# Optimization experiments

Measured on AMD Instinct MI355X. Metric: run time of the kernel, lower is better.

Reference implementation:

```python
import jax, jax.numpy as jnp
import numpy as np

N = 50000
E = 800000
NFEAT = 128
NHID = 64
NCLASS = 40


def setup_inputs() -> dict:
    key = jax.random.key(0)
    ks = jax.random.split(key, 12)
    return {
        "x": jax.random.normal(ks[0], (N, NFEAT), dtype=jnp.float32),
        "M": jax.random.uniform(ks[1], (N, 1), dtype=jnp.float32),
        "AM": jax.random.uniform(ks[2], (N, 1), dtype=jnp.float32),
        "adj_vals": jax.random.uniform(ks[3], (E,), dtype=jnp.float32),
        "adjZ_vals": jax.random.uniform(ks[4], (E,), dtype=jnp.float32),
        "W0": jax.random.normal(ks[5], (NFEAT, NFEAT), dtype=jnp.float32) * (1.414 / np.sqrt(NFEAT)),
        "b0": jnp.zeros((NFEAT,), dtype=jnp.float32),
        "W1": jax.random.normal(ks[6], (NFEAT, NHID), dtype=jnp.float32) * (1.414 / np.sqrt(NFEAT)),
        "b1": jnp.zeros((NHID,), dtype=jnp.float32),
        "W2": jax.random.normal(ks[7], (NHID, NCLASS), dtype=jnp.float32) * (1.0 / np.sqrt(NHID)),
        "b2": jnp.zeros((NCLASS,), dtype=jnp.float32),
        "row": jax.random.randint(ks[8], (E,), 0, N, dtype=jnp.int32),
        "col": jax.random.randint(ks[9], (E,), 0, N, dtype=jnp.int32),
    }


def _spmm(vals, row, col, X, n):
    # sparse (COO) @ dense: out[r] = sum_e vals[e] * X[col[e]] for row[e]==r
    return jax.ops.segment_sum(vals[:, None] * X[col], row, num_segments=n)


def reference(x, M, AM, adj_vals, adjZ_vals, W0, b0, W1, b1, W2, b2, row, col):
    n = x.shape[0]
    # gc0: PaGConv(nfeat->nfeat) on adjZ, then ReLU (dropout is identity in eval)
    h = _spmm(adjZ_vals, row, col, M * x, n) * AM
    h = jax.nn.relu(h @ W0 + b0)
    # gc1: PaGConv(nfeat->nhid) on adjZ, then ReLU
    h = _spmm(adjZ_vals, row, col, M * h, n) * AM
    h = jax.nn.relu(h @ W1 + b1)
    # gc2: plain GConv(nhid->nclass) on adj
    h = _spmm(adj_vals, row, col, h, n)
    h = h @ W2 + b2
    return jax.nn.log_softmax(h, axis=1)
```

## Files before the change

### kernel.cpp

```cpp
#include <hip/hip_runtime.h>
#include <hip/hip_bf16.h>
#include <math.h>


typedef __attribute__((ext_vector_type(8))) short bf16x8;
typedef __attribute__((ext_vector_type(4))) float f32x4;

#define HIST_EPB_LOG 14
#define HIST_EPB 16384
#define NBINS 50176

__device__ __forceinline__ float rl_f(float v, int j) {
    return __builtin_bit_cast(float,
        __builtin_amdgcn_readlane(__builtin_bit_cast(int, v), j));
}
__device__ __forceinline__ int rl_i(int v, int j) {
    return __builtin_amdgcn_readlane(v, j);
}
__device__ __forceinline__ unsigned short f2bf(float f) {
    unsigned u = __builtin_bit_cast(unsigned, f);
    u += 0x7fffu + ((u >> 16) & 1u);
    return (unsigned short)(u >> 16);
}
__device__ __forceinline__ unsigned pack2bf(float lo, float hi) {
    return (unsigned)f2bf(lo) | ((unsigned)f2bf(hi) << 16);
}
__device__ __forceinline__ float bf_lo(unsigned u) {
    return __builtin_bit_cast(float, u << 16);
}
__device__ __forceinline__ float bf_hi(unsigned u) {
    return __builtin_bit_cast(float, u & 0xffff0000u);
}
__device__ __forceinline__ float clampf(float v) {
    return fminf(fmaxf(v, -1e30f), 1e30f);
}


__global__ void prep_wt(const float* __restrict__ W0, const float* __restrict__ W1,
                        const float* __restrict__ W2,
                        unsigned short* __restrict__ wt0, unsigned short* __restrict__ wt1,
                        unsigned short* __restrict__ wt2) {
    int idx = blockIdx.x * 256 + threadIdx.x;
    if (idx < 128 * 128) {
        int nn = idx >> 7, k = idx & 127;
        wt0[idx] = f2bf(W0[k * 128 + nn]);
    }
    idx -= 128 * 128;
    if (idx >= 0 && idx < 64 * 128) {
        int nn = idx >> 7, k = idx & 127;
        wt1[idx] = f2bf(W1[k * 64 + nn]);
    }
    idx -= 64 * 128;
    if (idx >= 0 && idx < 48 * 64) {
        int nn = idx >> 6, k = idx & 63;
        wt2[idx] = (nn < 40) ? f2bf(W2[k * 40 + nn]) : (unsigned short)0;
    }
}


template <int K, int COLS, int NTPAD, bool ABF16, bool MSCALE>
__device__ __forceinline__ void gemm_mfma_body(const void* __restrict__ Asrc,
                                               const float* __restrict__ Mv,
                                               const unsigned short* __restrict__ Wt,
                                               unsigned short* __restrict__ outp,
                                               int n, int bid, int tid) {
    constexpr int KS = K / 32;
    const int lane = tid & 63;
    const int wid = tid >> 6;
    const int m15 = lane & 15;
    const int q = lane >> 4;
    const int rA = bid * 64 + wid * 16 + m15;

    bf16x8 a[KS];
    if constexpr (ABF16) {
        const unsigned short* A = (const unsigned short*)Asrc;
#pragma unroll
        for (int ks = 0; ks < KS; ++ks) {
            uint4 z = make_uint4(0u, 0u, 0u, 0u);
            if (rA < n) z = *(const uint4*)(A + (size_t)rA * K + ks * 32 + q * 8);
            a[ks] = __builtin_bit_cast(bf16x8, z);
        }
    } else {
        const float* A = (const float*)Asrc;
        float m = 1.0f;
        if constexpr (MSCALE) { if (rA < n) m = Mv[rA]; }
#pragma unroll
        for (int ks = 0; ks < KS; ++ks) {
            float4 lo = make_float4(0.f, 0.f, 0.f, 0.f);
            float4 hi = make_float4(0.f, 0.f, 0.f, 0.f);
            if (rA < n) {
                lo = *(const float4*)(A + (size_t)rA * K + ks * 32 + q * 8);
                hi = *(const float4*)(A + (size_t)rA * K + ks * 32 + q * 8 + 4);
            }
            union { bf16x8 v; unsigned short u[8]; } pk;
            pk.u[0] = f2bf(lo.x * m); pk.u[1] = f2bf(lo.y * m);
            pk.u[2] = f2bf(lo.z * m); pk.u[3] = f2bf(lo.w * m);
            pk.u[4] = f2bf(hi.x * m); pk.u[5] = f2bf(hi.y * m);
            pk.u[6] = f2bf(hi.z * m); pk.u[7] = f2bf(hi.w * m);
            a[ks] = pk.v;
        }
    }

#pragma unroll
    for (int nt = 0; nt < NTPAD / 16; ++nt) {
        f32x4 acc = {0.f, 0.f, 0.f, 0.f};
        const int bn = nt * 16 + m15;
#pragma unroll
        for (int ks = 0; ks < KS; ++ks) {
            const uint4 z = *(const uint4*)(Wt + (size_t)bn * K + ks * 32 + q * 8);
            const bf16x8 b = __builtin_bit_cast(bf16x8, z);
            acc = __builtin_amdgcn_mfma_f32_16x16x32_bf16(a[ks], b, acc, 0, 0, 0);
        }
        const int gc = nt * 16 + m15;
#pragma unroll
        for (int rr = 0; rr < 4; ++rr) {
            const int gr = bid * 64 + wid * 16 + q * 4 + rr;
            bool ok = gr < n;
            if constexpr (NTPAD != COLS) ok = ok && (gc < COLS);
            if (ok) outp[(size_t)gr * COLS + gc] = f2bf(clampf(acc[rr]));
        }
    }
}

template <int K, int COLS, int NTPAD, bool ABF16, bool MSCALE>
__launch_bounds__(256)
__global__ void gemm_mfma(const void* __restrict__ A, const float* __restrict__ Mv,
                          const unsigned short* __restrict__ Wt,
                          unsigned short* __restrict__ out, int n) {
    gemm_mfma_body<K, COLS, NTPAD, ABF16, MSCALE>(A, Mv, Wt, out, n, blockIdx.x,
                                                  threadIdx.x);
}


__launch_bounds__(1024)
__global__ void hist_gemm0(const int* __restrict__ row,
                           unsigned short* __restrict__ cntmat,
                           unsigned short* __restrict__ lrank, int E, int NB,
                           const float* __restrict__ x, const float* __restrict__ Mv,
                           const unsigned short* __restrict__ Wt0,
                           unsigned short* __restrict__ t_buf, int n) {
    __shared__ unsigned hcnt[NBINS / 2];
    const int blk = blockIdx.x;
    const int t = threadIdx.x;
    if (blk < NB) {
        for (int i = t; i < NBINS / 2; i += 1024) hcnt[i] = 0u;
        __syncthreads();
        const int s = blk << HIST_EPB_LOG;
        const int e = min(E, s + HIST_EPB);
        for (int i = s + t; i < e; i += 1024) {
            const int r = row[i];
            const unsigned sh = (unsigned)(r & 1) << 4;
            const unsigned old = atomicAdd(&hcnt[r >> 1], 1u << sh);
            lrank[i] = (unsigned short)((old >> sh) & 0xffffu);
        }
        __syncthreads();
        unsigned* dst = (unsigned*)(cntmat + (size_t)blk * NBINS);
        for (int i = t; i < NBINS / 2; i += 1024) dst[i] = hcnt[i];
    } else {
        const int sub = t >> 8;
        gemm_mfma_body<128, 128, 128, false, true>(x, Mv, Wt0, t_buf, n,
                                                   (blk - NB) * 4 + sub, t & 255);
    }
}


__global__ void scan_part2(unsigned short* __restrict__ cm, int* __restrict__ rp,
                           int* __restrict__ bsums, int n, int NB) {
    __shared__ int sdata[256];
    const int t = threadIdx.x;
    const int base = blockIdx.x * 1024 + t * 4;
    unsigned r0 = 0, r1 = 0, r2 = 0, r3 = 0;
    for (int b = 0; b < NB; ++b) {
        uint2* p = (uint2*)&cm[(size_t)b * NBINS + base];
        const uint2 c = *p;
        uint2 o;
        o.x = r0 | (r1 << 16);
        o.y = r2 | (r3 << 16);
        *p = o;
        r0 += c.x & 0xffffu; r1 += c.x >> 16;
        r2 += c.y & 0xffffu; r3 += c.y >> 16;
    }
    int v[4] = {(int)r0, (int)r1, (int)r2, (int)r3};
    const int tsum = v[0] + v[1] + v[2] + v[3];
    sdata[t] = tsum;
    __syncthreads();
    for (int off = 1; off < 256; off <<= 1) {
        int xv = (t >= off) ? sdata[t - off] : 0;
        __syncthreads();
        sdata[t] += xv;
        __syncthreads();
    }
    int run = sdata[t] - tsum;
    if (t == 255) bsums[blockIdx.x] = sdata[t];
#pragma unroll
    for (int i = 0; i < 4; ++i) {
        if (base + i < n) rp[base + i] = run;
        run += v[i];
    }
}

__global__ void scan_top(int* __restrict__ bs, int nb) {
    int t = threadIdx.x;
    int orig = (t < nb) ? bs[t] : 0;
    int v = orig;
#pragma unroll
    for (int off = 1; off < 64; off <<= 1) {
        int x = __shfl_up(v, off);
        if (t >= off) v += x;
    }
    if (t < nb) bs[t] = v - orig;
}

__global__ void scan_add(int* __restrict__ rp, const int* __restrict__ bs,
                         int n, int total) {
    int i = blockIdx.x * blockDim.x + threadIdx.x;
    if (i < n) rp[i] += bs[i >> 10];
    if (i == 0) rp[n] = total;
}


__global__ void scatter_kernel(const int* __restrict__ row, const int* __restrict__ col,
                               const float* __restrict__ vA, const float* __restrict__ vZ,
                               const int* __restrict__ rp,
                               const unsigned short* __restrict__ cm,
                               const unsigned short* __restrict__ lrank,
                               float* __restrict__ packed, int E) {
    int e = blockIdx.x * blockDim.x + threadIdx.x;
    if (e >= E) return;
    const int r = row[e];
    const int pos = rp[r] + (int)cm[(size_t)(e >> HIST_EPB_LOG) * NBINS + r]
                          + (int)lrank[e];
    float3 pk;
    pk.x = __int_as_float(col[e]);
    pk.y = vZ[e];
    pk.z = vA[e];
    *(float3*)&packed[(size_t)3 * pos] = pk;
}


__launch_bounds__(256)
__global__ void spmm128_kernel(const float* __restrict__ packed,
                               const int* __restrict__ rp, const unsigned short* __restrict__ X,
                               const float* __restrict__ AM, const float* __restrict__ Mv,
                               const float* __restrict__ bias,
                               unsigned short* __restrict__ out, int n) {
    const int lane = threadIdx.x & 63;
    const int r = (int)((blockIdx.x * (unsigned)blockDim.x + threadIdx.x) >> 6);
    if (r >= n) return;
    const int s = __builtin_amdgcn_readfirstlane(rp[r]);
    const int e = __builtin_amdgcn_readfirstlane(rp[r + 1]);

    float acc0 = 0.0f, acc1 = 0.0f;
    for (int base = s; base < e; base += 64) {
        const int nn = min(64, e - base);
        int ci = 0; float vf = 0.0f;
        if (lane < nn) {
            const float3 pk = *(const float3*)&packed[(size_t)3 * (base + lane)];
            ci = __builtin_bit_cast(int, pk.x);
            vf = pk.y;
        }
        int j = 0;
        for (; j + 8 <= nn; j += 8) {
            unsigned u[8];
#pragma unroll
            for (int q = 0; q < 8; ++q) {
                const int cq = rl_i(ci, j + q);
                u[q] = *(const unsigned*)(X + (size_t)cq * 128 + lane * 2);
            }
#pragma unroll
            for (int q = 0; q < 8; ++q) {
                const float vq = rl_f(vf, j + q);
                acc0 += vq * bf_lo(u[q]);
                acc1 += vq * bf_hi(u[q]);
            }
        }
        for (; j < nn; ++j) {
            const int cq = rl_i(ci, j);
            const float vq = rl_f(vf, j);
            const unsigned u = *(const unsigned*)(X + (size_t)cq * 128 + lane * 2);
            acc0 += vq * bf_lo(u);
            acc1 += vq * bf_hi(u);
        }
    }

    const float am = AM[r];
    const float mr = Mv[r];
    const float o0 = fminf(fmaxf((acc0 * am + bias[2 * lane]) * mr, 0.0f), 1e30f);
    const float o1 = fminf(fmaxf((acc1 * am + bias[2 * lane + 1]) * mr, 0.0f), 1e30f);
    ((unsigned*)out)[(size_t)r * 64 + lane] = pack2bf(o0, o1);
}


__launch_bounds__(256)
__global__ void spmm64_kernel(const float* __restrict__ packed,
                              const int* __restrict__ rp, const unsigned short* __restrict__ X,
                              const float* __restrict__ AM, const float* __restrict__ bias,
                              unsigned short* __restrict__ out, int n) {
    const int lane = threadIdx.x & 63;
    const int g = lane >> 5;
    const int ls = lane & 31;
    const int r = (int)((blockIdx.x * (unsigned)blockDim.x + threadIdx.x) >> 6);
    if (r >= n) return;
    const int s = __builtin_amdgcn_readfirstlane(rp[r]);
    const int e = __builtin_amdgcn_readfirstlane(rp[r + 1]);

    float acc0 = 0.0f, acc1 = 0.0f;
    for (int base = s; base < e; base += 64) {
        const int nn = min(64, e - base);
        int ci = 0; float vf = 0.0f;
        if (lane < nn) {
            const float3 pk = *(const float3*)&packed[(size_t)3 * (base + lane)];
            ci = __builtin_bit_cast(int, pk.x);
            vf = pk.y;
        }
        for (int j = 0; j < nn; j += 8) {
#pragma unroll
            for (int q = 0; q < 4; ++q) {
                const int jj = j + 2 * q + g;
                const bool ok = jj < nn;
                const int idx = jj & 63;
                const int c = __shfl(ci, idx);
                const float v = __shfl(vf, idx);
                if (ok) {
                    const unsigned u = *(const unsigned*)(X + (size_t)c * 64 + ls * 2);
                    acc0 += v * bf_lo(u);
                    acc1 += v * bf_hi(u);
                }
            }
        }
    }
    acc0 += __shfl_xor(acc0, 32);
    acc1 += __shfl_xor(acc1, 32);

    if (lane < 32) {
        const float am = AM[r];
        const float o0 = fminf(fmaxf(acc0 * am + bias[2 * ls], 0.0f), 1e30f);
        const float o1 = fminf(fmaxf(acc1 * am + bias[2 * ls + 1], 0.0f), 1e30f);
        ((unsigned*)out)[(size_t)r * 32 + ls] = pack2bf(o0, o1);
    }
}


__launch_bounds__(256)
__global__ void spmm40_kernel(const float* __restrict__ packed,
                              const int* __restrict__ rp, const unsigned short* __restrict__ X,
                              const float* __restrict__ bias,
                              float* __restrict__ out, int n) {
    const int lane = threadIdx.x & 63;
    const int g = lane / 20;
    const int ls = lane - 20 * g;
    const bool active = g < 3;
    const int r = (int)((blockIdx.x * (unsigned)blockDim.x + threadIdx.x) >> 6);
    if (r >= n) return;
    const int s = __builtin_amdgcn_readfirstlane(rp[r]);
    const int e = __builtin_amdgcn_readfirstlane(rp[r + 1]);

    float acc0 = 0.0f, acc1 = 0.0f;
    for (int base = s; base < e; base += 64) {
        const int nn = min(64, e - base);
        int ci = 0; float vf = 0.0f;
        if (lane < nn) {
            const float3 pk = *(const float3*)&packed[(size_t)3 * (base + lane)];
            ci = __builtin_bit_cast(int, pk.x);
            vf = pk.z;
        }
        for (int j = 0; j < nn; j += 12) {
#pragma unroll
            for (int q = 0; q < 4; ++q) {
                const int jj = j + 3 * q + g;
                const bool ok = active && jj < nn;
                const int idx = jj & 63;
                const int c = __shfl(ci, idx);
                const float v = __shfl(vf, idx);
                if (ok) {
                    const unsigned u = *(const unsigned*)(X + (size_t)c * 40 + ls * 2);
                    acc0 += v * bf_lo(u);
                    acc1 += v * bf_hi(u);
                }
            }
        }
    }
    {
        const float a1 = __shfl(acc0, (lane + 20) & 63);
        const float a2 = __shfl(acc0, (lane + 40) & 63);
        const float b1 = __shfl(acc1, (lane + 20) & 63);
        const float b2 = __shfl(acc1, (lane + 40) & 63);
        acc0 += a1 + a2;
        acc1 += b1 + b2;
    }

    const bool own = lane < 20;
    const float vv0 = own ? fminf(fmaxf(acc0 + bias[2 * ls], -1e30f), 1e30f) : -INFINITY;
    const float vv1 = own ? fminf(fmaxf(acc1 + bias[2 * ls + 1], -1e30f), 1e30f) : -INFINITY;
    float mx = fmaxf(vv0, vv1);
#pragma unroll
    for (int off = 32; off > 0; off >>= 1) mx = fmaxf(mx, __shfl_xor(mx, off));
    float sum = own ? (expf(vv0 - mx) + expf(vv1 - mx)) : 0.0f;
#pragma unroll
    for (int off = 32; off > 0; off >>= 1) sum += __shfl_xor(sum, off);
    if (own) {
        const float lse = mx + logf(sum);
        *(float2*)(out + (size_t)r * 40 + ls * 2) = make_float2(vv0 - lse, vv1 - lse);
    }
}


extern "C" void kernel_launch(void* const* d_in, const int* in_sizes, int n_in,
                              void* d_out, int out_size, void* d_ws, size_t ws_size,
                              hipStream_t stream) {
    const float* x    = (const float*)d_in[0];
    const float* M    = (const float*)d_in[1];
    const float* AM   = (const float*)d_in[2];
    const float* adjv = (const float*)d_in[3];
    const float* adjZ = (const float*)d_in[4];
    const float* W0   = (const float*)d_in[5];
    const float* b0   = (const float*)d_in[6];
    const float* W1   = (const float*)d_in[7];
    const float* b1   = (const float*)d_in[8];
    const float* W2   = (const float*)d_in[9];
    const float* b2   = (const float*)d_in[10];
    const int* row    = (const int*)d_in[11];
    const int* col    = (const int*)d_in[12];
    float* out = (float*)d_out;

    const int n = in_sizes[1];
    const int E = in_sizes[3];

    float* t_f   = (float*)d_ws;
    unsigned short* t_buf = (unsigned short*)t_f;
    unsigned short* wt0 = t_buf + (size_t)n * 128;
    unsigned short* wt1 = wt0 + 128 * 128;
    unsigned short* wt2 = wt1 + 64 * 128;
    float* h_f   = t_f + (size_t)n * 128;
    unsigned short* h_buf = (unsigned short*)h_f;
    unsigned short* lrank  = (unsigned short*)h_f;
    unsigned short* cntmat = lrank + (size_t)E;
    int* rp      = (int*)(h_f + (size_t)n * 128);
    int* bsums   = rp + (n + 1);
    float* packed = (float*)(bsums + 64);

    const int NB = (E + HIST_EPB - 1) >> HIST_EPB_LOG;
    const int gemmBlocks = (n + 63) / 64;
    const int gemmB4 = (gemmBlocks + 3) / 4;

    prep_wt<<<(128 * 128 + 64 * 128 + 48 * 64 + 255) / 256, 256, 0, stream>>>(
        W0, W1, W2, wt0, wt1, wt2);

    hist_gemm0<<<NB + gemmB4, 1024, 0, stream>>>(row, cntmat, lrank, E, NB,
                                                 x, M, wt0, t_buf, n);

    const int nblk = (n + 1023) >> 10;
    scan_part2<<<nblk, 256, 0, stream>>>(cntmat, rp, bsums, n, NB);
    scan_top<<<1, 64, 0, stream>>>(bsums, nblk);
    scan_add<<<(n + 255) / 256, 256, 0, stream>>>(rp, bsums, n, E);
    scatter_kernel<<<(E + 255) / 256, 256, 0, stream>>>(row, col, adjv, adjZ, rp,
                                                        cntmat, lrank, packed, E);

    const int spmmBlocks = (n + 3) / 4;

    spmm128_kernel<<<spmmBlocks, 256, 0, stream>>>(packed, rp, t_buf, AM, M, b0, h_buf, n);
    gemm_mfma<128, 64, 64, true, false><<<gemmBlocks, 256, 0, stream>>>(h_buf, nullptr, wt1,
                                                                        t_buf, n);
    spmm64_kernel<<<spmmBlocks, 256, 0, stream>>>(packed, rp, t_buf, AM, b1, h_buf, n);
    gemm_mfma<64, 40, 48, true, false><<<gemmBlocks, 256, 0, stream>>>(h_buf, nullptr, wt2,
                                                                       t_buf, n);
    spmm40_kernel<<<spmmBlocks, 256, 0, stream>>>(packed, rp, t_buf, b2, out, n);
}
```

Baseline: 273.9 us.

## Merge scan stages into absolute offsets and widen SpMM gather batches

Replaces the three-kernel scan (part2/top/add) with a sum kernel plus a finishing kernel. The finishing kernel computes per-block absolute row offsets into a new 32-bit cmabs array, so scatter does a single lookup instead of adding rp and the relative count. Separately, the 128-wide SpMM gets a 16-deep gather unroll, the 64-wide SpMM has each lane load 8 bytes across four row groups, and the 40-wide SpMM doubles its unroll. These trade one kernel launch and scatter-side loads for an extra 4-byte-per-entry offset matrix write and higher register pressure in the SpMM kernels.

```diff
diff --git a/kernel.cpp b/kernel.cpp
--- a/kernel.cpp
+++ b/kernel.cpp
@@ -164,23 +164,18 @@
 }
 
 
-__global__ void scan_part2(unsigned short* __restrict__ cm, int* __restrict__ rp,
-                           int* __restrict__ bsums, int n, int NB) {
+__global__ void scan_sum(const unsigned short* __restrict__ cm, int* __restrict__ rp,
+                         int* __restrict__ bsums, int n, int NB) {
     __shared__ int sdata[256];
     const int t = threadIdx.x;
     const int base = blockIdx.x * 1024 + t * 4;
-    unsigned r0 = 0, r1 = 0, r2 = 0, r3 = 0;
+    unsigned s0 = 0, s1 = 0, s2 = 0, s3 = 0;
     for (int b = 0; b < NB; ++b) {
-        uint2* p = (uint2*)&cm[(size_t)b * NBINS + base];
-        const uint2 c = *p;
-        uint2 o;
-        o.x = r0 | (r1 << 16);
-        o.y = r2 | (r3 << 16);
-        *p = o;
-        r0 += c.x & 0xffffu; r1 += c.x >> 16;
-        r2 += c.y & 0xffffu; r3 += c.y >> 16;
-    }
-    int v[4] = {(int)r0, (int)r1, (int)r2, (int)r3};
+        const uint2 c = *(const uint2*)&cm[(size_t)b * NBINS + base];
+        s0 += c.x & 0xffffu; s1 += c.x >> 16;
+        s2 += c.y & 0xffffu; s3 += c.y >> 16;
+    }
+    int v[4] = {(int)s0, (int)s1, (int)s2, (int)s3};
     const int tsum = v[0] + v[1] + v[2] + v[3];
     sdata[t] = tsum;
     __syncthreads();
@@ -199,37 +194,39 @@
     }
 }
 
-__global__ void scan_top(int* __restrict__ bs, int nb) {
-    int t = threadIdx.x;
-    int orig = (t < nb) ? bs[t] : 0;
-    int v = orig;
-#pragma unroll
-    for (int off = 1; off < 64; off <<= 1) {
-        int x = __shfl_up(v, off);
-        if (t >= off) v += x;
-    }
-    if (t < nb) bs[t] = v - orig;
-}
-
-__global__ void scan_add(int* __restrict__ rp, const int* __restrict__ bs,
-                         int n, int total) {
-    int i = blockIdx.x * blockDim.x + threadIdx.x;
-    if (i < n) rp[i] += bs[i >> 10];
-    if (i == 0) rp[n] = total;
+
+__launch_bounds__(256)
+__global__ void scan_fin(const unsigned short* __restrict__ cm,
+                         unsigned* __restrict__ cmabs, int* __restrict__ rp,
+                         const int* __restrict__ bsums, int n, int NB, int E) {
+    const int lane = threadIdx.x & 63;
+    const int myblk = blockIdx.x >> 2;
+    int bv = (lane < myblk) ? bsums[lane] : 0;
+#pragma unroll
+    for (int off = 32; off; off >>= 1) bv += __shfl_xor(bv, off);
+    const int i = blockIdx.x * 256 + threadIdx.x;
+    if (i < n) {
+        int run = rp[i] + bv;
+        rp[i] = run;
+        for (int b = 0; b < NB; ++b) {
+            cmabs[(size_t)b * NBINS + i] = (unsigned)run;
+            run += (int)cm[(size_t)b * NBINS + i];
+        }
+    }
+    if (blockIdx.x == 0 && threadIdx.x == 0) rp[n] = E;
 }
 
 
 __global__ void scatter_kernel(const int* __restrict__ row, const int* __restrict__ col,
                                const float* __restrict__ vA, const float* __restrict__ vZ,
-                               const int* __restrict__ rp,
-                               const unsigned short* __restrict__ cm,
+                               const unsigned* __restrict__ cmabs,
                                const unsigned short* __restrict__ lrank,
                                float* __restrict__ packed, int E) {
     int e = blockIdx.x * blockDim.x + threadIdx.x;
     if (e >= E) return;
     const int r = row[e];
-    const int pos = rp[r] + (int)cm[(size_t)(e >> HIST_EPB_LOG) * NBINS + r]
-                          + (int)lrank[e];
+    const int pos = (int)(cmabs[(size_t)(e >> HIST_EPB_LOG) * NBINS + r]
+                          + (unsigned)lrank[e]);
     float3 pk;
     pk.x = __int_as_float(col[e]);
     pk.y = vZ[e];
@@ -260,6 +257,20 @@
             vf = pk.y;
         }
         int j = 0;
+        for (; j + 16 <= nn; j += 16) {
+            unsigned u[16];
+#pragma unroll
+            for (int q = 0; q < 16; ++q) {
+                const int cq = rl_i(ci, j + q);
+                u[q] = *(const unsigned*)(X + (size_t)cq * 128 + lane * 2);
+            }
+#pragma unroll
+            for (int q = 0; q < 16; ++q) {
+                const float vq = rl_f(vf, j + q);
+                acc0 += vq * bf_lo(u[q]);
+                acc1 += vq * bf_hi(u[q]);
+            }
+        }
         for (; j + 8 <= nn; j += 8) {
             unsigned u[8];
 #pragma unroll
@@ -297,14 +308,14 @@
                               const float* __restrict__ AM, const float* __restrict__ bias,
                               unsigned short* __restrict__ out, int n) {
     const int lane = threadIdx.x & 63;
-    const int g = lane >> 5;
-    const int ls = lane & 31;
+    const int g = lane >> 4;
+    const int ls = lane & 15;
     const int r = (int)((blockIdx.x * (unsigned)blockDim.x + threadIdx.x) >> 6);
     if (r >= n) return;
     const int s = __builtin_amdgcn_readfirstlane(rp[r]);
     const int e = __builtin_amdgcn_readfirstlane(rp[r + 1]);
 
-    float acc0 = 0.0f, acc1 = 0.0f;
+    float a0 = 0.0f, a1 = 0.0f, a2 = 0.0f, a3 = 0.0f;
     for (int base = s; base < e; base += 64) {
         const int nn = min(64, e - base);
         int ci = 0; float vf = 0.0f;
@@ -313,30 +324,39 @@
             ci = __builtin_bit_cast(int, pk.x);
             vf = pk.y;
         }
-        for (int j = 0; j < nn; j += 8) {
+        for (int j = 0; j < nn; j += 16) {
 #pragma unroll
             for (int q = 0; q < 4; ++q) {
-                const int jj = j + 2 * q + g;
+                const int jj = j + 4 * q + g;
                 const bool ok = jj < nn;
                 const int idx = jj & 63;
                 const int c = __shfl(ci, idx);
                 const float v = __shfl(vf, idx);
                 if (ok) {
-                    const unsigned u = *(const unsigned*)(X + (size_t)c * 64 + ls * 2);
-                    acc0 += v * bf_lo(u);
-                    acc1 += v * bf_hi(u);
+                    const uint2 u = *(const uint2*)(X + (size_t)c * 64 + ls * 4);
+                    a0 += v * bf_lo(u.x);
+                    a1 += v * bf_hi(u.x);
+                    a2 += v * bf_lo(u.y);
+                    a3 += v * bf_hi(u.y);
                 }
             }
         }
     }
-    acc0 += __shfl_xor(acc0, 32);
-    acc1 += __shfl_xor(acc1, 32);
-
-    if (lane < 32) {
+    a0 += __shfl_xor(a0, 16); a0 += __shfl_xor(a0, 32);
+    a1 += __shfl_xor(a1, 16); a1 += __shfl_xor(a1, 32);
+    a2 += __shfl_xor(a2, 16); a2 += __shfl_xor(a2, 32);
+    a3 += __shfl_xor(a3, 16); a3 += __shfl_xor(a3, 32);
+
+    if (lane < 16) {
         const float am = AM[r];
-        const float o0 = fminf(fmaxf(acc0 * am + bias[2 * ls], 0.0f), 1e30f);
-        const float o1 = fminf(fmaxf(acc1 * am + bias[2 * ls + 1], 0.0f), 1e30f);
-        ((unsigned*)out)[(size_t)r * 32 + ls] = pack2bf(o0, o1);
+        const float o0 = fminf(fmaxf(a0 * am + bias[4 * ls + 0], 0.0f), 1e30f);
+        const float o1 = fminf(fmaxf(a1 * am + bias[4 * ls + 1], 0.0f), 1e30f);
+        const float o2 = fminf(fmaxf(a2 * am + bias[4 * ls + 2], 0.0f), 1e30f);
+        const float o3 = fminf(fmaxf(a3 * am + bias[4 * ls + 3], 0.0f), 1e30f);
+        uint2 w;
+        w.x = pack2bf(o0, o1);
+        w.y = pack2bf(o2, o3);
+        *(uint2*)((unsigned*)out + (size_t)r * 32 + ls * 2) = w;
     }
 }
 
@@ -364,9 +384,9 @@
             ci = __builtin_bit_cast(int, pk.x);
             vf = pk.z;
         }
-        for (int j = 0; j < nn; j += 12) {
-#pragma unroll
-            for (int q = 0; q < 4; ++q) {
+        for (int j = 0; j < nn; j += 24) {
+#pragma unroll
+            for (int q = 0; q < 8; ++q) {
                 const int jj = j + 3 * q + g;
                 const bool ok = active && jj < nn;
                 const int idx = jj & 63;
@@ -435,6 +455,7 @@
     unsigned short* h_buf = (unsigned short*)h_f;
     unsigned short* lrank  = (unsigned short*)h_f;
     unsigned short* cntmat = lrank + (size_t)E;
+    unsigned* cmabs = (unsigned*)(cntmat + (size_t)64 * NBINS);
     int* rp      = (int*)(h_f + (size_t)n * 128);
     int* bsums   = rp + (n + 1);
     float* packed = (float*)(bsums + 64);
@@ -450,11 +471,10 @@
                                                  x, M, wt0, t_buf, n);
 
     const int nblk = (n + 1023) >> 10;
-    scan_part2<<<nblk, 256, 0, stream>>>(cntmat, rp, bsums, n, NB);
-    scan_top<<<1, 64, 0, stream>>>(bsums, nblk);
-    scan_add<<<(n + 255) / 256, 256, 0, stream>>>(rp, bsums, n, E);
-    scatter_kernel<<<(E + 255) / 256, 256, 0, stream>>>(row, col, adjv, adjZ, rp,
-                                                        cntmat, lrank, packed, E);
+    scan_sum<<<nblk, 256, 0, stream>>>(cntmat, rp, bsums, n, NB);
+    scan_fin<<<(n + 255) / 256, 256, 0, stream>>>(cntmat, cmabs, rp, bsums, n, NB, E);
+    scatter_kernel<<<(E + 255) / 256, 256, 0, stream>>>(row, col, adjv, adjZ,
+                                                        cmabs, lrank, packed, E);
 
     const int spmmBlocks = (n + 3) / 4;
 
```

Measured after the change: 278.3 us. Within noise of the previous version (+1.6%).
